# Optimization experiments

Measured on AMD Instinct MI355X. Metric: run time of the kernel, lower is better.

The kernel has to match this reference:

```python
import jax, jax.numpy as jnp
import numpy as np

NUM_USERS = 100000
NUM_ITEMS = 100000
DIM = 128
B = 8192
H = 200
ATTN_HID = 64


def setup_inputs() -> dict:
    key = jax.random.key(0)
    ks = jax.random.split(key, 10)
    user_ids = jax.random.randint(ks[0], (B,), 0, NUM_USERS)
    item_ids = jax.random.randint(ks[1], (B,), 0, NUM_ITEMS)
    user_history = jax.random.randint(ks[2], (B, H), 0, NUM_ITEMS)
    user_table = jax.random.normal(ks[3], (NUM_USERS, DIM), dtype=jnp.float32)
    item_table = jax.random.normal(ks[4], (NUM_ITEMS, DIM), dtype=jnp.float32)
    feature_interaction = jax.random.normal(ks[5], (DIM, DIM), dtype=jnp.float32)
    # attention MLP: Linear(2*DIM, 64) -> ReLU -> Linear(64, 1) -> Sigmoid
    lim1 = 1.0 / np.sqrt(2 * DIM)
    w1 = jax.random.uniform(ks[6], (2 * DIM, ATTN_HID), minval=-lim1, maxval=lim1, dtype=jnp.float32)
    b1 = jax.random.uniform(ks[7], (ATTN_HID,), minval=-lim1, maxval=lim1, dtype=jnp.float32)
    lim2 = 1.0 / np.sqrt(ATTN_HID)
    w2 = jax.random.uniform(ks[8], (ATTN_HID, 1), minval=-lim2, maxval=lim2, dtype=jnp.float32)
    b2 = jax.random.uniform(ks[9], (1,), minval=-lim2, maxval=lim2, dtype=jnp.float32)
    return {
        "user_ids": user_ids,
        "item_ids": item_ids,
        "user_history": user_history,
        "user_table": user_table,
        "item_table": item_table,
        "feature_interaction": feature_interaction,
        "w1": w1,
        "b1": b1,
        "w2": w2,
        "b2": b2,
    }


def reference(user_ids, item_ids, user_history, user_table, item_table,
              feature_interaction, w1, b1, w2, b2):
    user_emb = user_table[user_ids]          # [B, D]
    item_emb = item_table[item_ids]          # [B, D]
    # bilinear interaction: (user_emb @ W) . item_emb, summed over D -> [B, 1]
    interaction = jnp.sum((user_emb @ feature_interaction) * item_emb, axis=1, keepdims=True)
    # attention-weighted history pooling
    history_emb = item_table[user_history]   # [B, H, D]
    u = jnp.broadcast_to(user_emb[:, None, :], history_emb.shape)  # [B, H, D]
    attn_in = jnp.concatenate([u, history_emb], axis=-1)           # [B, H, 2D]
    h = jax.nn.relu(attn_in @ w1 + b1)                             # [B, H, 64]
    attn_w = jax.nn.sigmoid(h @ w2 + b2)                           # [B, H, 1]
    history_repr = jnp.sum(attn_w * history_emb, axis=1)           # [B, D]
    user_out = user_emb + history_repr
    return (user_out, item_emb, interaction)
```

## Files before the change

### kernel.cpp

```cpp
#include <hip/hip_runtime.h>
#include <math.h>

#define NB      8192
#define HLEN    200
#define DIM     128
#define AH      64
#define NITEMS  100000
#define NTILE   13
#define INTER_BLKS (NB / 32)

typedef __attribute__((ext_vector_type(4))) float f32x4;
typedef __attribute__((ext_vector_type(2))) float f32x2;
typedef __attribute__((ext_vector_type(4))) int   i32x4;
typedef __attribute__((ext_vector_type(8))) short bf16x8;
typedef unsigned int uint;

__device__ __forceinline__ unsigned short f2bf(float f) {
  uint u = __float_as_uint(f);
  u += 0x7fffu + ((u >> 16) & 1u);
  return (unsigned short)(u >> 16);
}
__device__ __forceinline__ float bf2f(unsigned short h) {
  return __uint_as_float(((uint)h) << 16);
}
__device__ __forceinline__ long pick64(const i32x4& v, int h) {
  return (long)(unsigned)v[2 * h] | ((long)(unsigned)v[2 * h + 1] << 32);
}
__device__ __forceinline__ i32x4 ldnt(const void* p) {
  return __builtin_nontemporal_load((const i32x4*)p);
}

__global__ __launch_bounds__(256)
void pre_kernel(const int* __restrict__ user_ids,
                const int* __restrict__ item_ids,
                const float* __restrict__ user_table,
                const float* __restrict__ item_table,
                const float* __restrict__ fi,
                const float* __restrict__ w1,
                unsigned char* __restrict__ tbl8,
                unsigned char* __restrict__ w1f8,
                float* __restrict__ out_item,
                float* __restrict__ out_inter) {
  const int t = threadIdx.x;
  if (blockIdx.x < INTER_BLKS) {
    __shared__ unsigned short fitb[DIM * 130];
    __shared__ float u4[4][DIM];
    __shared__ float red[4][4];
    for (int i = t; i < DIM * DIM; i += 256) {
      int d = i >> 7, e = i & 127;
      fitb[e * 130 + d] = f2bf(fi[i]);
    }
    const int col = t & 127;
    const int dh = t >> 7;
    const int lane = t & 63;
    const int wv = t >> 6;
    const int b0 = blockIdx.x * 32;
    const unsigned short* fr = &fitb[col * 130 + dh * 64];
    for (int grp = 0; grp < 8; ++grp) {
      __syncthreads();
      for (int i = t; i < 4 * DIM; i += 256) {
        int bi = i >> 7, d = i & 127;
        u4[bi][d] = user_table[(long)user_ids[b0 + grp * 4 + bi] * DIM + d];
      }
      __syncthreads();
      float a0 = 0.f, a1 = 0.f, a2 = 0.f, a3 = 0.f;
#pragma unroll 4
      for (int d = 0; d < 64; d += 4) {
        float f0 = bf2f(fr[d]), f1 = bf2f(fr[d + 1]), f2 = bf2f(fr[d + 2]), f3 = bf2f(fr[d + 3]);
        f32x4 q0 = *(const f32x4*)&u4[0][dh * 64 + d];
        f32x4 q1 = *(const f32x4*)&u4[1][dh * 64 + d];
        f32x4 q2 = *(const f32x4*)&u4[2][dh * 64 + d];
        f32x4 q3 = *(const f32x4*)&u4[3][dh * 64 + d];
        a0 = fmaf(f0, q0[0], a0); a0 = fmaf(f1, q0[1], a0); a0 = fmaf(f2, q0[2], a0); a0 = fmaf(f3, q0[3], a0);
        a1 = fmaf(f0, q1[0], a1); a1 = fmaf(f1, q1[1], a1); a1 = fmaf(f2, q1[2], a1); a1 = fmaf(f3, q1[3], a1);
        a2 = fmaf(f0, q2[0], a2); a2 = fmaf(f1, q2[1], a2); a2 = fmaf(f2, q2[2], a2); a2 = fmaf(f3, q2[3], a2);
        a3 = fmaf(f0, q3[0], a3); a3 = fmaf(f1, q3[1], a3); a3 = fmaf(f2, q3[2], a3); a3 = fmaf(f3, q3[3], a3);
      }
      const int bb = b0 + grp * 4;
      const float vv0 = item_table[(long)item_ids[bb + 0] * DIM + col];
      const float vv1 = item_table[(long)item_ids[bb + 1] * DIM + col];
      const float vv2 = item_table[(long)item_ids[bb + 2] * DIM + col];
      const float vv3 = item_table[(long)item_ids[bb + 3] * DIM + col];
      if (dh == 0) {
        out_item[(long)(bb + 0) * DIM + col] = vv0;
        out_item[(long)(bb + 1) * DIM + col] = vv1;
        out_item[(long)(bb + 2) * DIM + col] = vv2;
        out_item[(long)(bb + 3) * DIM + col] = vv3;
      }
      float p0 = a0 * vv0, p1 = a1 * vv1, p2 = a2 * vv2, p3 = a3 * vv3;
#pragma unroll
      for (int msk = 1; msk <= 32; msk <<= 1) {
        p0 += __shfl_xor(p0, msk);
        p1 += __shfl_xor(p1, msk);
        p2 += __shfl_xor(p2, msk);
        p3 += __shfl_xor(p3, msk);
      }
      if (lane == 0) { red[wv][0] = p0; red[wv][1] = p1; red[wv][2] = p2; red[wv][3] = p3; }
      __syncthreads();
      if (t < 4)
        out_inter[bb + t] = red[0][t] + red[1][t] + red[2][t] + red[3][t];
    }
  } else {
    const int cb = blockIdx.x - INTER_BLKS;
    const int cgrid = gridDim.x - INTER_BLKS;
    const long t0 = (long)cb * 256 + t;
    const long total4 = (long)NITEMS * DIM / 4;
    const long stride = (long)cgrid * 256;
    for (long i = t0; i < total4; i += stride) {
      f32x4 v = ((const f32x4*)item_table)[i];
      int p = __builtin_amdgcn_cvt_pk_fp8_f32(v[0], v[1], 0, false);
      p     = __builtin_amdgcn_cvt_pk_fp8_f32(v[2], v[3], p, true);
      ((int*)tbl8)[i] = p;
    }
    if (t0 < 16384) {
      int L = (int)t0;
      int j = L & 7, gg = (L >> 3) & 3, mm = (L >> 5) & 15;
      int nt = (L >> 9) & 3, s = (L >> 11) & 3, part = (L >> 13) & 1;
      int kg = part * 128 + (s >> 1) * 64 + gg * 16 + (s & 1) * 8 + j;
      float v = w1[kg * AH + nt * 16 + mm];
      int pk = __builtin_amdgcn_cvt_pk_fp8_f32(v, v, 0, false);
      w1f8[L] = (unsigned char)(pk & 0xff);
    }
  }
}

__global__ __launch_bounds__(256)
void main_kernel_fp8(const int* __restrict__ user_ids,
                     const int* __restrict__ user_history,
                     const float* __restrict__ user_table,
                     const unsigned char* __restrict__ tbl8,
                     const unsigned char* __restrict__ w1f8,
                     const float* __restrict__ b1,
                     const float* __restrict__ w2,
                     const float* __restrict__ b2,
                     float* __restrict__ out_user) {
  const int lane = threadIdx.x & 63;
  const int wave = threadIdx.x >> 6;
  const int b = blockIdx.x * 4 + wave;
  const int m = lane & 15;
  const int g = lane >> 4;

  const int uid = __builtin_amdgcn_readfirstlane(user_ids[b]);
  const float* urow = user_table + (long)uid * DIM;
  const int* hrow = user_history + (long)b * HLEN;

  int idxs[NTILE];
#pragma unroll
  for (int t = 0; t < NTILE; ++t) {
    int row = t * 16 + m;
    idxs[t] = (row < HLEN) ? hrow[row] : 0;
  }

  i32x4 pa[5][2];
#define LOADT(T, BUF)                                                          \
  {                                                                            \
    const unsigned char* p_ = tbl8 + ((long)idxs[T] << 7) + g * 16;            \
    pa[BUF][0] = ldnt(p_);                                                     \
    pa[BUF][1] = ldnt(p_ + 64);                                                \
  }
  LOADT(0, 0) LOADT(1, 1) LOADT(2, 2) LOADT(3, 3)

  i32x4 uf[2];
#pragma unroll
  for (int kb = 0; kb < 2; ++kb) {
    const float* up = urow + kb * 64 + g * 16;
    f32x4 q0 = *(const f32x4*)(up + 0);
    f32x4 q1 = *(const f32x4*)(up + 4);
    f32x4 q2 = *(const f32x4*)(up + 8);
    f32x4 q3 = *(const f32x4*)(up + 12);
    i32x4 d;
    d[0] = __builtin_amdgcn_cvt_pk_fp8_f32(q0[0], q0[1], 0, false);
    d[0] = __builtin_amdgcn_cvt_pk_fp8_f32(q0[2], q0[3], d[0], true);
    d[1] = __builtin_amdgcn_cvt_pk_fp8_f32(q1[0], q1[1], 0, false);
    d[1] = __builtin_amdgcn_cvt_pk_fp8_f32(q1[2], q1[3], d[1], true);
    d[2] = __builtin_amdgcn_cvt_pk_fp8_f32(q2[0], q2[1], 0, false);
    d[2] = __builtin_amdgcn_cvt_pk_fp8_f32(q2[2], q2[3], d[2], true);
    d[3] = __builtin_amdgcn_cvt_pk_fp8_f32(q3[0], q3[1], 0, false);
    d[3] = __builtin_amdgcn_cvt_pk_fp8_f32(q3[2], q3[3], d[3], true);
    uf[kb] = d;
  }

  const unsigned char* wtop = w1f8;
  const unsigned char* wbot = w1f8 + 8192;

  f32x4 accu[4];
#pragma unroll
  for (int nt = 0; nt < 4; ++nt) accu[nt] = (f32x4){0.f, 0.f, 0.f, 0.f};
#pragma unroll
  for (int s = 0; s < 4; ++s) {
    long a_s = pick64(uf[s >> 1], s & 1);
#pragma unroll
    for (int nt = 0; nt < 4; ++nt) {
      long bf = *(const long*)(wtop + ((s * 4 + nt) * 16 + m) * 32 + g * 8);
      accu[nt] = __builtin_amdgcn_mfma_f32_16x16x32_fp8_fp8(a_s, bf, accu[nt], 0, 0, 0);
    }
  }
  float ubreg[4], w2reg[4];
#pragma unroll
  for (int nt = 0; nt < 4; ++nt) {
    ubreg[nt] = accu[nt][0] + b1[nt * 16 + m];
    w2reg[nt] = w2[nt * 16 + m];
  }
  const float b2v = b2[0];

  long bfr[4][4];
#pragma unroll
  for (int s = 0; s < 4; ++s)
#pragma unroll
    for (int nt = 0; nt < 4; ++nt)
      bfr[s][nt] = *(const long*)(wbot + ((s * 4 + nt) * 16 + m) * 32 + g * 8);

  float arep[32];
#pragma unroll
  for (int c = 0; c < 32; ++c) arep[c] = 0.f;

#pragma unroll
  for (int t = 0; t < NTILE; ++t) {
    if (t + 4 < NTILE) LOADT(t + 4, (t + 4) % 5)
    const int cb = t % 5;

    f32x4 acc[4];
#pragma unroll
    for (int nt = 0; nt < 4; ++nt) acc[nt] = (f32x4){0.f, 0.f, 0.f, 0.f};
#pragma unroll
    for (int s = 0; s < 4; ++s) {
      long a_s = pick64(pa[cb][s >> 1], s & 1);
#pragma unroll
      for (int nt = 0; nt < 4; ++nt)
        acc[nt] = __builtin_amdgcn_mfma_f32_16x16x32_fp8_fp8(a_s, bfr[s][nt], acc[nt], 0, 0, 0);
    }

    float sums[4];
#pragma unroll
    for (int r = 0; r < 4; ++r) {
      float s = 0.f;
#pragma unroll
      for (int nt = 0; nt < 4; ++nt) {
        float h = fmaxf(acc[nt][r] + ubreg[nt], 0.f);
        s = fmaf(h, w2reg[nt], s);
      }
      s += __shfl_xor(s, 1);
      s += __shfl_xor(s, 2);
      s += __shfl_xor(s, 4);
      s += __shfl_xor(s, 8);
      sums[r] = s;
    }
    const int q = m & 3;
    float keep = (q == 0) ? sums[0] : (q == 1) ? sums[1] : (q == 2) ? sums[2] : sums[3];
    float sv = __shfl(keep, ((m >> 2) << 4) | m);
    float attw = 1.f / (1.f + __expf(-(sv + b2v)));
    if (t * 16 + m >= HLEN) attw = 0.f;

#pragma unroll
    for (int kb = 0; kb < 2; ++kb)
#pragma unroll
      for (int d = 0; d < 4; ++d) {
        f32x2 lo = __builtin_amdgcn_cvt_pk_f32_fp8(pa[cb][kb][d], false);
        f32x2 hi = __builtin_amdgcn_cvt_pk_f32_fp8(pa[cb][kb][d], true);
        const int base = kb * 16 + d * 4;
        arep[base + 0] = fmaf(attw, lo[0], arep[base + 0]);
        arep[base + 1] = fmaf(attw, lo[1], arep[base + 1]);
        arep[base + 2] = fmaf(attw, hi[0], arep[base + 2]);
        arep[base + 3] = fmaf(attw, hi[1], arep[base + 3]);
      }
  }
#undef LOADT

#pragma unroll
  for (int c = 0; c < 32; ++c) {
    arep[c] += __shfl_xor(arep[c], 1);
    arep[c] += __shfl_xor(arep[c], 2);
    arep[c] += __shfl_xor(arep[c], 4);
    arep[c] += __shfl_xor(arep[c], 8);
  }
  if (m == 0) {
#pragma unroll
    for (int kb = 0; kb < 2; ++kb)
#pragma unroll
      for (int i4 = 0; i4 < 4; ++i4) {
        const int col = kb * 64 + g * 16 + i4 * 4;
        f32x4 uv = *(const f32x4*)(urow + col);
        f32x4 o;
#pragma unroll
        for (int qq = 0; qq < 4; ++qq) o[qq] = uv[qq] + arep[kb * 16 + i4 * 4 + qq];
        *(f32x4*)(out_user + (long)b * DIM + col) = o;
      }
  }
}

__global__ __launch_bounds__(256)
void main_fallback(const int* __restrict__ user_ids,
                   const int* __restrict__ user_history,
                   const float* __restrict__ user_table,
                   const float* __restrict__ item_table,
                   const float* __restrict__ w1,
                   const float* __restrict__ b1,
                   const float* __restrict__ w2,
                   const float* __restrict__ b2,
                   float* __restrict__ out_user) {
  const int lane = threadIdx.x & 63;
  const int wave = threadIdx.x >> 6;
  const int b = blockIdx.x * 4 + wave;
  const int m = lane & 15, g = lane >> 4;
  const int uid = __builtin_amdgcn_readfirstlane(user_ids[b]);
  const float* urow = user_table + (long)uid * DIM;
  float upj = b1[lane];
#pragma unroll 8
  for (int d = 0; d < DIM; ++d) upj = fmaf(urow[d], w1[d * AH + lane], upj);
  bf16x8 bfr[4][4];
#pragma unroll
  for (int ks = 0; ks < 4; ++ks)
#pragma unroll
    for (int nt = 0; nt < 4; ++nt) {
      bf16x8 bv;
#pragma unroll
      for (int j = 0; j < 8; ++j)
        bv[j] = (short)f2bf(w1[(DIM + ks * 32 + g * 8 + j) * AH + nt * 16 + m]);
      bfr[ks][nt] = bv;
    }
  float ubreg[4], w2reg[4];
#pragma unroll
  for (int nt = 0; nt < 4; ++nt) {
    ubreg[nt] = __shfl(upj, nt * 16 + m);
    w2reg[nt] = w2[nt * 16 + m];
  }
  const float b2v = b2[0];
  float arep[32];
#pragma unroll
  for (int c = 0; c < 32; ++c) arep[c] = 0.f;
  const int* hrow = user_history + (long)b * HLEN;
  for (int t = 0; t < NTILE; ++t) {
    const int row = t * 16 + m;
    const int idx = (row < HLEN) ? hrow[row] : 0;
    bf16x8 a[4];
    const float* rp = item_table + (long)idx * DIM;
#pragma unroll
    for (int ks = 0; ks < 4; ++ks) {
      f32x4 lo = *(const f32x4*)(rp + ks * 32 + g * 8);
      f32x4 hi = *(const f32x4*)(rp + ks * 32 + g * 8 + 4);
      bf16x8 av;
      av[0] = (short)f2bf(lo[0]); av[1] = (short)f2bf(lo[1]);
      av[2] = (short)f2bf(lo[2]); av[3] = (short)f2bf(lo[3]);
      av[4] = (short)f2bf(hi[0]); av[5] = (short)f2bf(hi[1]);
      av[6] = (short)f2bf(hi[2]); av[7] = (short)f2bf(hi[3]);
      a[ks] = av;
    }
    f32x4 acc[4];
#pragma unroll
    for (int nt = 0; nt < 4; ++nt) acc[nt] = (f32x4){0.f, 0.f, 0.f, 0.f};
#pragma unroll
    for (int ks = 0; ks < 4; ++ks)
#pragma unroll
      for (int nt = 0; nt < 4; ++nt)
        acc[nt] = __builtin_amdgcn_mfma_f32_16x16x32_bf16(a[ks], bfr[ks][nt], acc[nt], 0, 0, 0);
    float sums[4];
#pragma unroll
    for (int r = 0; r < 4; ++r) {
      float s = 0.f;
#pragma unroll
      for (int nt = 0; nt < 4; ++nt) {
        float h = fmaxf(acc[nt][r] + ubreg[nt], 0.f);
        s = fmaf(h, w2reg[nt], s);
      }
      s += __shfl_xor(s, 1); s += __shfl_xor(s, 2);
      s += __shfl_xor(s, 4); s += __shfl_xor(s, 8);
      sums[r] = s;
    }
    const int q = m & 3;
    float keep = (q == 0) ? sums[0] : (q == 1) ? sums[1] : (q == 2) ? sums[2] : sums[3];
    float sv = __shfl(keep, ((m >> 2) << 4) | m);
    float attw = 1.f / (1.f + __expf(-(sv + b2v)));
    if (row >= HLEN) attw = 0.f;
#pragma unroll
    for (int ks = 0; ks < 4; ++ks)
#pragma unroll
      for (int j = 0; j < 8; ++j)
        arep[ks * 8 + j] = fmaf(attw, bf2f((unsigned short)a[ks][j]), arep[ks * 8 + j]);
  }
#pragma unroll
  for (int c = 0; c < 32; ++c) {
    arep[c] += __shfl_xor(arep[c], 1);
    arep[c] += __shfl_xor(arep[c], 2);
    arep[c] += __shfl_xor(arep[c], 4);
    arep[c] += __shfl_xor(arep[c], 8);
  }
  if (m == 0) {
#pragma unroll
    for (int ks = 0; ks < 4; ++ks)
#pragma unroll
      for (int j = 0; j < 8; ++j) {
        const int col = ks * 32 + g * 8 + j;
        out_user[(long)b * DIM + col] = urow[col] + arep[ks * 8 + j];
      }
  }
}

extern "C" void kernel_launch(void* const* d_in, const int* in_sizes, int n_in,
                              void* d_out, int out_size, void* d_ws, size_t ws_size,
                              hipStream_t stream) {
  const int*   user_ids     = (const int*)d_in[0];
  const int*   item_ids     = (const int*)d_in[1];
  const int*   user_history = (const int*)d_in[2];
  const float* user_table   = (const float*)d_in[3];
  const float* item_table   = (const float*)d_in[4];
  const float* fi           = (const float*)d_in[5];
  const float* w1           = (const float*)d_in[6];
  const float* b1           = (const float*)d_in[7];
  const float* w2           = (const float*)d_in[8];
  const float* b2           = (const float*)d_in[9];

  float* out       = (float*)d_out;
  float* out_user  = out;
  float* out_item  = out + (size_t)NB * DIM;
  float* out_inter = out + (size_t)2 * NB * DIM;

  const size_t need = (size_t)NITEMS * DIM + 16384;
  if (ws_size >= need) {
    unsigned char* tbl8 = (unsigned char*)d_ws;
    unsigned char* w1f8 = tbl8 + (size_t)NITEMS * DIM;
    pre_kernel<<<INTER_BLKS + 1024, 256, 0, stream>>>(user_ids, item_ids, user_table,
        item_table, fi, w1, tbl8, w1f8, out_item, out_inter);
    main_kernel_fp8<<<NB / 4, 256, 0, stream>>>(user_ids, user_history, user_table,
        tbl8, w1f8, b1, w2, b2, out_user);
  } else {
    main_fallback<<<NB / 4, 256, 0, stream>>>(user_ids, user_history, user_table,
        item_table, w1, b1, w2, b2, out_user);
    pre_kernel<<<INTER_BLKS, 256, 0, stream>>>(user_ids, item_ids, user_table,
        item_table, fi, w1, nullptr, nullptr, out_item, out_inter);
  }
}
```

Measured before the change: 109.1 us.

## Stage history gathers into LDS via async global_load_lds with explicit waitcnt pipeline

The main kernel now gathers the fp8 history rows straight into a swizzled, 5-deep per-wave LDS ring using global_load_lds, instead of holding them in registers. Consumption is paced by explicit vmcnt waits, and loads are issued as each tile is consumed. This frees VGPRs and overlaps the gathers with MFMA work. W1 fragments and biases are hoisted up front, and b1 is folded into the accumulator init. The pre-kernel now uses one block per 4 batch rows instead of 32, so the interaction blocks each rebuild the transposed bf16 feature matrix in LDS, which adds redundant preload work.

```diff
diff --git a/kernel.cpp b/kernel.cpp
--- a/kernel.cpp
+++ b/kernel.cpp
@@ -7,7 +7,8 @@
 #define AH      64
 #define NITEMS  100000
 #define NTILE   13
-#define INTER_BLKS (NB / 32)
+#define GRP_BLKS (NB / 4)
+#define CONV_BLKS 1024
 
 typedef __attribute__((ext_vector_type(4))) float f32x4;
 typedef __attribute__((ext_vector_type(2))) float f32x2;
@@ -26,8 +27,10 @@
 __device__ __forceinline__ long pick64(const i32x4& v, int h) {
   return (long)(unsigned)v[2 * h] | ((long)(unsigned)v[2 * h + 1] << 32);
 }
-__device__ __forceinline__ i32x4 ldnt(const void* p) {
-  return __builtin_nontemporal_load((const i32x4*)p);
+__device__ __forceinline__ void gld16(const unsigned char* g, unsigned char* l) {
+  __builtin_amdgcn_global_load_lds(
+      (const __attribute__((address_space(1))) unsigned int*)g,
+      (__attribute__((address_space(3))) unsigned int*)l, 16, 0, 0);
 }
 
 __global__ __launch_bounds__(256)
@@ -42,7 +45,7 @@
                 float* __restrict__ out_item,
                 float* __restrict__ out_inter) {
   const int t = threadIdx.x;
-  if (blockIdx.x < INTER_BLKS) {
+  if (blockIdx.x < GRP_BLKS) {
     __shared__ unsigned short fitb[DIM * 130];
     __shared__ float u4[4][DIM];
     __shared__ float red[4][4];
@@ -54,58 +57,53 @@
     const int dh = t >> 7;
     const int lane = t & 63;
     const int wv = t >> 6;
-    const int b0 = blockIdx.x * 32;
+    const int bb = blockIdx.x * 4;
+    for (int i = t; i < 4 * DIM; i += 256) {
+      int bi = i >> 7, d = i & 127;
+      u4[bi][d] = user_table[(long)user_ids[bb + bi] * DIM + d];
+    }
+    __syncthreads();
     const unsigned short* fr = &fitb[col * 130 + dh * 64];
-    for (int grp = 0; grp < 8; ++grp) {
-      __syncthreads();
-      for (int i = t; i < 4 * DIM; i += 256) {
-        int bi = i >> 7, d = i & 127;
-        u4[bi][d] = user_table[(long)user_ids[b0 + grp * 4 + bi] * DIM + d];
-      }
-      __syncthreads();
-      float a0 = 0.f, a1 = 0.f, a2 = 0.f, a3 = 0.f;
+    float a0 = 0.f, a1 = 0.f, a2 = 0.f, a3 = 0.f;
 #pragma unroll 4
-      for (int d = 0; d < 64; d += 4) {
-        float f0 = bf2f(fr[d]), f1 = bf2f(fr[d + 1]), f2 = bf2f(fr[d + 2]), f3 = bf2f(fr[d + 3]);
-        f32x4 q0 = *(const f32x4*)&u4[0][dh * 64 + d];
-        f32x4 q1 = *(const f32x4*)&u4[1][dh * 64 + d];
-        f32x4 q2 = *(const f32x4*)&u4[2][dh * 64 + d];
-        f32x4 q3 = *(const f32x4*)&u4[3][dh * 64 + d];
-        a0 = fmaf(f0, q0[0], a0); a0 = fmaf(f1, q0[1], a0); a0 = fmaf(f2, q0[2], a0); a0 = fmaf(f3, q0[3], a0);
-        a1 = fmaf(f0, q1[0], a1); a1 = fmaf(f1, q1[1], a1); a1 = fmaf(f2, q1[2], a1); a1 = fmaf(f3, q1[3], a1);
-        a2 = fmaf(f0, q2[0], a2); a2 = fmaf(f1, q2[1], a2); a2 = fmaf(f2, q2[2], a2); a2 = fmaf(f3, q2[3], a2);
-        a3 = fmaf(f0, q3[0], a3); a3 = fmaf(f1, q3[1], a3); a3 = fmaf(f2, q3[2], a3); a3 = fmaf(f3, q3[3], a3);
-      }
-      const int bb = b0 + grp * 4;
-      const float vv0 = item_table[(long)item_ids[bb + 0] * DIM + col];
-      const float vv1 = item_table[(long)item_ids[bb + 1] * DIM + col];
-      const float vv2 = item_table[(long)item_ids[bb + 2] * DIM + col];
-      const float vv3 = item_table[(long)item_ids[bb + 3] * DIM + col];
-      if (dh == 0) {
-        out_item[(long)(bb + 0) * DIM + col] = vv0;
-        out_item[(long)(bb + 1) * DIM + col] = vv1;
-        out_item[(long)(bb + 2) * DIM + col] = vv2;
-        out_item[(long)(bb + 3) * DIM + col] = vv3;
-      }
-      float p0 = a0 * vv0, p1 = a1 * vv1, p2 = a2 * vv2, p3 = a3 * vv3;
-#pragma unroll
-      for (int msk = 1; msk <= 32; msk <<= 1) {
-        p0 += __shfl_xor(p0, msk);
-        p1 += __shfl_xor(p1, msk);
-        p2 += __shfl_xor(p2, msk);
-        p3 += __shfl_xor(p3, msk);
-      }
-      if (lane == 0) { red[wv][0] = p0; red[wv][1] = p1; red[wv][2] = p2; red[wv][3] = p3; }
-      __syncthreads();
-      if (t < 4)
-        out_inter[bb + t] = red[0][t] + red[1][t] + red[2][t] + red[3][t];
-    }
+    for (int d = 0; d < 64; d += 4) {
+      float f0 = bf2f(fr[d]), f1 = bf2f(fr[d + 1]), f2 = bf2f(fr[d + 2]), f3 = bf2f(fr[d + 3]);
+      f32x4 q0 = *(const f32x4*)&u4[0][dh * 64 + d];
+      f32x4 q1 = *(const f32x4*)&u4[1][dh * 64 + d];
+      f32x4 q2 = *(const f32x4*)&u4[2][dh * 64 + d];
+      f32x4 q3 = *(const f32x4*)&u4[3][dh * 64 + d];
+      a0 = fmaf(f0, q0[0], a0); a0 = fmaf(f1, q0[1], a0); a0 = fmaf(f2, q0[2], a0); a0 = fmaf(f3, q0[3], a0);
+      a1 = fmaf(f0, q1[0], a1); a1 = fmaf(f1, q1[1], a1); a1 = fmaf(f2, q1[2], a1); a1 = fmaf(f3, q1[3], a1);
+      a2 = fmaf(f0, q2[0], a2); a2 = fmaf(f1, q2[1], a2); a2 = fmaf(f2, q2[2], a2); a2 = fmaf(f3, q2[3], a2);
+      a3 = fmaf(f0, q3[0], a3); a3 = fmaf(f1, q3[1], a3); a3 = fmaf(f2, q3[2], a3); a3 = fmaf(f3, q3[3], a3);
+    }
+    const float vv0 = item_table[(long)item_ids[bb + 0] * DIM + col];
+    const float vv1 = item_table[(long)item_ids[bb + 1] * DIM + col];
+    const float vv2 = item_table[(long)item_ids[bb + 2] * DIM + col];
+    const float vv3 = item_table[(long)item_ids[bb + 3] * DIM + col];
+    if (dh == 0) {
+      out_item[(long)(bb + 0) * DIM + col] = vv0;
+      out_item[(long)(bb + 1) * DIM + col] = vv1;
+      out_item[(long)(bb + 2) * DIM + col] = vv2;
+      out_item[(long)(bb + 3) * DIM + col] = vv3;
+    }
+    float p0 = a0 * vv0, p1 = a1 * vv1, p2 = a2 * vv2, p3 = a3 * vv3;
+#pragma unroll
+    for (int msk = 1; msk <= 32; msk <<= 1) {
+      p0 += __shfl_xor(p0, msk);
+      p1 += __shfl_xor(p1, msk);
+      p2 += __shfl_xor(p2, msk);
+      p3 += __shfl_xor(p3, msk);
+    }
+    if (lane == 0) { red[wv][0] = p0; red[wv][1] = p1; red[wv][2] = p2; red[wv][3] = p3; }
+    __syncthreads();
+    if (t < 4)
+      out_inter[bb + t] = red[0][t] + red[1][t] + red[2][t] + red[3][t];
   } else {
-    const int cb = blockIdx.x - INTER_BLKS;
-    const int cgrid = gridDim.x - INTER_BLKS;
+    const int cb = blockIdx.x - GRP_BLKS;
     const long t0 = (long)cb * 256 + t;
     const long total4 = (long)NITEMS * DIM / 4;
-    const long stride = (long)cgrid * 256;
+    const long stride = (long)CONV_BLKS * 256;
     for (long i = t0; i < total4; i += stride) {
       f32x4 v = ((const f32x4*)item_table)[i];
       int p = __builtin_amdgcn_cvt_pk_fp8_f32(v[0], v[1], 0, false);
@@ -134,11 +132,13 @@
                      const float* __restrict__ w2,
                      const float* __restrict__ b2,
                      float* __restrict__ out_user) {
+  __shared__ unsigned char stg[4][5 * 2048];
   const int lane = threadIdx.x & 63;
   const int wave = threadIdx.x >> 6;
   const int b = blockIdx.x * 4 + wave;
   const int m = lane & 15;
   const int g = lane >> 4;
+  unsigned char* mystg = &stg[wave][0];
 
   const int uid = __builtin_amdgcn_readfirstlane(user_ids[b]);
   const float* urow = user_table + (long)uid * DIM;
@@ -151,37 +151,56 @@
     idxs[t] = (row < HLEN) ? hrow[row] : 0;
   }
 
-  i32x4 pa[5][2];
-#define LOADT(T, BUF)                                                          \
-  {                                                                            \
-    const unsigned char* p_ = tbl8 + ((long)idxs[T] << 7) + g * 16;            \
-    pa[BUF][0] = ldnt(p_);                                                     \
-    pa[BUF][1] = ldnt(p_ + 64);                                                \
-  }
-  LOADT(0, 0) LOADT(1, 1) LOADT(2, 2) LOADT(3, 3)
-
-  i32x4 uf[2];
-#pragma unroll
-  for (int kb = 0; kb < 2; ++kb) {
-    const float* up = urow + kb * 64 + g * 16;
-    f32x4 q0 = *(const f32x4*)(up + 0);
-    f32x4 q1 = *(const f32x4*)(up + 4);
-    f32x4 q2 = *(const f32x4*)(up + 8);
-    f32x4 q3 = *(const f32x4*)(up + 12);
-    i32x4 d;
-    d[0] = __builtin_amdgcn_cvt_pk_fp8_f32(q0[0], q0[1], 0, false);
-    d[0] = __builtin_amdgcn_cvt_pk_fp8_f32(q0[2], q0[3], d[0], true);
-    d[1] = __builtin_amdgcn_cvt_pk_fp8_f32(q1[0], q1[1], 0, false);
-    d[1] = __builtin_amdgcn_cvt_pk_fp8_f32(q1[2], q1[3], d[1], true);
-    d[2] = __builtin_amdgcn_cvt_pk_fp8_f32(q2[0], q2[1], 0, false);
-    d[2] = __builtin_amdgcn_cvt_pk_fp8_f32(q2[2], q2[3], d[2], true);
-    d[3] = __builtin_amdgcn_cvt_pk_fp8_f32(q3[0], q3[1], 0, false);
-    d[3] = __builtin_amdgcn_cvt_pk_fp8_f32(q3[2], q3[3], d[3], true);
-    uf[kb] = d;
-  }
+  f32x4 uq[8];
+#pragma unroll
+  for (int kb = 0; kb < 2; ++kb)
+#pragma unroll
+    for (int j = 0; j < 4; ++j)
+      uq[kb * 4 + j] = *(const f32x4*)(urow + kb * 64 + g * 16 + 4 * j);
 
   const unsigned char* wtop = w1f8;
   const unsigned char* wbot = w1f8 + 8192;
+  long wt[4][4], bfr[4][4];
+#pragma unroll
+  for (int s = 0; s < 4; ++s)
+#pragma unroll
+    for (int nt = 0; nt < 4; ++nt) {
+      wt[s][nt]  = *(const long*)(wtop + ((s * 4 + nt) * 16 + m) * 32 + g * 8);
+      bfr[s][nt] = *(const long*)(wbot + ((s * 4 + nt) * 16 + m) * 32 + g * 8);
+    }
+  float b1reg[4], w2reg[4];
+#pragma unroll
+  for (int nt = 0; nt < 4; ++nt) {
+    b1reg[nt] = b1[nt * 16 + m];
+    w2reg[nt] = w2[nt * 16 + m];
+  }
+  const float b2v = b2[0];
+
+  const unsigned swg = (unsigned)(((lane & 7) ^ (lane >> 3)) << 4);
+#define LOADT(T)                                                               \
+  {                                                                            \
+    int r0_ = __shfl(idxs[T], lane >> 3);                                      \
+    int r1_ = __shfl(idxs[T], 8 + (lane >> 3));                                \
+    unsigned char* l0_ = mystg + ((T) % 5) * 2048;                             \
+    gld16(tbl8 + ((long)r0_ << 7) + swg, l0_);                                 \
+    gld16(tbl8 + ((long)r1_ << 7) + swg, l0_ + 1024);                          \
+  }
+  LOADT(0) LOADT(1) LOADT(2) LOADT(3) LOADT(4)
+
+  i32x4 uf[2];
+#pragma unroll
+  for (int kb = 0; kb < 2; ++kb) {
+    i32x4 d;
+    d[0] = __builtin_amdgcn_cvt_pk_fp8_f32(uq[kb*4+0][0], uq[kb*4+0][1], 0, false);
+    d[0] = __builtin_amdgcn_cvt_pk_fp8_f32(uq[kb*4+0][2], uq[kb*4+0][3], d[0], true);
+    d[1] = __builtin_amdgcn_cvt_pk_fp8_f32(uq[kb*4+1][0], uq[kb*4+1][1], 0, false);
+    d[1] = __builtin_amdgcn_cvt_pk_fp8_f32(uq[kb*4+1][2], uq[kb*4+1][3], d[1], true);
+    d[2] = __builtin_amdgcn_cvt_pk_fp8_f32(uq[kb*4+2][0], uq[kb*4+2][1], 0, false);
+    d[2] = __builtin_amdgcn_cvt_pk_fp8_f32(uq[kb*4+2][2], uq[kb*4+2][3], d[2], true);
+    d[3] = __builtin_amdgcn_cvt_pk_fp8_f32(uq[kb*4+3][0], uq[kb*4+3][1], 0, false);
+    d[3] = __builtin_amdgcn_cvt_pk_fp8_f32(uq[kb*4+3][2], uq[kb*4+3][3], d[3], true);
+    uf[kb] = d;
+  }
 
   f32x4 accu[4];
 #pragma unroll
@@ -190,80 +209,83 @@
   for (int s = 0; s < 4; ++s) {
     long a_s = pick64(uf[s >> 1], s & 1);
 #pragma unroll
-    for (int nt = 0; nt < 4; ++nt) {
-      long bf = *(const long*)(wtop + ((s * 4 + nt) * 16 + m) * 32 + g * 8);
-      accu[nt] = __builtin_amdgcn_mfma_f32_16x16x32_fp8_fp8(a_s, bf, accu[nt], 0, 0, 0);
-    }
-  }
-  float ubreg[4], w2reg[4];
-#pragma unroll
-  for (int nt = 0; nt < 4; ++nt) {
-    ubreg[nt] = accu[nt][0] + b1[nt * 16 + m];
-    w2reg[nt] = w2[nt * 16 + m];
-  }
-  const float b2v = b2[0];
-
-  long bfr[4][4];
-#pragma unroll
-  for (int s = 0; s < 4; ++s)
-#pragma unroll
     for (int nt = 0; nt < 4; ++nt)
-      bfr[s][nt] = *(const long*)(wbot + ((s * 4 + nt) * 16 + m) * 32 + g * 8);
+      accu[nt] = __builtin_amdgcn_mfma_f32_16x16x32_fp8_fp8(a_s, wt[s][nt], accu[nt], 0, 0, 0);
+  }
+  float ubreg[4];
+#pragma unroll
+  for (int nt = 0; nt < 4; ++nt) ubreg[nt] = accu[nt][0] + b1reg[nt];
 
   float arep[32];
 #pragma unroll
   for (int c = 0; c < 32; ++c) arep[c] = 0.f;
 
-#pragma unroll
-  for (int t = 0; t < NTILE; ++t) {
-    if (t + 4 < NTILE) LOADT(t + 4, (t + 4) % 5)
-    const int cb = t % 5;
-
-    f32x4 acc[4];
-#pragma unroll
-    for (int nt = 0; nt < 4; ++nt) acc[nt] = (f32x4){0.f, 0.f, 0.f, 0.f};
-#pragma unroll
-    for (int s = 0; s < 4; ++s) {
-      long a_s = pick64(pa[cb][s >> 1], s & 1);
-#pragma unroll
-      for (int nt = 0; nt < 4; ++nt)
-        acc[nt] = __builtin_amdgcn_mfma_f32_16x16x32_fp8_fp8(a_s, bfr[s][nt], acc[nt], 0, 0, 0);
-    }
-
-    float sums[4];
-#pragma unroll
-    for (int r = 0; r < 4; ++r) {
-      float s = 0.f;
-#pragma unroll
-      for (int nt = 0; nt < 4; ++nt) {
-        float h = fmaxf(acc[nt][r] + ubreg[nt], 0.f);
-        s = fmaf(h, w2reg[nt], s);
-      }
-      s += __shfl_xor(s, 1);
-      s += __shfl_xor(s, 2);
-      s += __shfl_xor(s, 4);
-      s += __shfl_xor(s, 8);
-      sums[r] = s;
-    }
-    const int q = m & 3;
-    float keep = (q == 0) ? sums[0] : (q == 1) ? sums[1] : (q == 2) ? sums[2] : sums[3];
-    float sv = __shfl(keep, ((m >> 2) << 4) | m);
-    float attw = 1.f / (1.f + __expf(-(sv + b2v)));
-    if (t * 16 + m >= HLEN) attw = 0.f;
-
-#pragma unroll
-    for (int kb = 0; kb < 2; ++kb)
-#pragma unroll
-      for (int d = 0; d < 4; ++d) {
-        f32x2 lo = __builtin_amdgcn_cvt_pk_f32_fp8(pa[cb][kb][d], false);
-        f32x2 hi = __builtin_amdgcn_cvt_pk_f32_fp8(pa[cb][kb][d], true);
-        const int base = kb * 16 + d * 4;
-        arep[base + 0] = fmaf(attw, lo[0], arep[base + 0]);
-        arep[base + 1] = fmaf(attw, lo[1], arep[base + 1]);
-        arep[base + 2] = fmaf(attw, hi[0], arep[base + 2]);
-        arep[base + 3] = fmaf(attw, hi[1], arep[base + 3]);
-      }
-  }
+  const unsigned sw0 = (unsigned)((g ^ (m & 7)) << 4);
+
+#define STEP(T, WN, ISS)                                                       \
+  {                                                                            \
+    asm volatile("s_waitcnt vmcnt(" WN ")" ::: "memory");                      \
+    __builtin_amdgcn_sched_barrier(0);                                         \
+    const unsigned char* rp_ = mystg + ((T) % 5) * 2048 + (m << 7);            \
+    i32x4 pa0 = *(const i32x4*)(rp_ + sw0);                                    \
+    i32x4 pa1 = *(const i32x4*)(rp_ + (sw0 ^ 64));                             \
+    f32x4 acc[4];                                                              \
+    _Pragma("unroll")                                                          \
+    for (int nt = 0; nt < 4; ++nt)                                             \
+      acc[nt] = (f32x4){ubreg[nt], ubreg[nt], ubreg[nt], ubreg[nt]};           \
+    _Pragma("unroll")                                                          \
+    for (int s = 0; s < 4; ++s) {                                              \
+      long a_s = pick64((s < 2) ? pa0 : pa1, s & 1);                           \
+      _Pragma("unroll")                                                        \
+      for (int nt = 0; nt < 4; ++nt)                                           \
+        acc[nt] = __builtin_amdgcn_mfma_f32_16x16x32_fp8_fp8(a_s, bfr[s][nt], acc[nt], 0, 0, 0); \
+    }                                                                          \
+    float sums[4];                                                             \
+    _Pragma("unroll")                                                          \
+    for (int r = 0; r < 4; ++r) {                                              \
+      float s_ = fmaxf(acc[0][r], 0.f) * w2reg[0];                             \
+      s_ = fmaf(fmaxf(acc[1][r], 0.f), w2reg[1], s_);                          \
+      s_ = fmaf(fmaxf(acc[2][r], 0.f), w2reg[2], s_);                          \
+      s_ = fmaf(fmaxf(acc[3][r], 0.f), w2reg[3], s_);                          \
+      s_ += __shfl_xor(s_, 1);                                                 \
+      s_ += __shfl_xor(s_, 2);                                                 \
+      s_ += __shfl_xor(s_, 4);                                                 \
+      s_ += __shfl_xor(s_, 8);                                                 \
+      sums[r] = s_;                                                            \
+    }                                                                          \
+    const int q_ = m & 3;                                                      \
+    float keep_ = (q_ == 0) ? sums[0] : (q_ == 1) ? sums[1]                    \
+                 : (q_ == 2) ? sums[2] : sums[3];                              \
+    float sv_ = __shfl(keep_, ((m >> 2) << 4) | m);                            \
+    float attw = 1.f / (1.f + __expf(-(sv_ + b2v)));                           \
+    if ((T) * 16 + m >= HLEN) attw = 0.f;                                      \
+    _Pragma("unroll")                                                          \
+    for (int d = 0; d < 4; ++d) {                                              \
+      f32x2 lo0 = __builtin_amdgcn_cvt_pk_f32_fp8(pa0[d], false);              \
+      f32x2 hi0 = __builtin_amdgcn_cvt_pk_f32_fp8(pa0[d], true);               \
+      arep[d * 4 + 0] = fmaf(attw, lo0[0], arep[d * 4 + 0]);                   \
+      arep[d * 4 + 1] = fmaf(attw, lo0[1], arep[d * 4 + 1]);                   \
+      arep[d * 4 + 2] = fmaf(attw, hi0[0], arep[d * 4 + 2]);                   \
+      arep[d * 4 + 3] = fmaf(attw, hi0[1], arep[d * 4 + 3]);                   \
+      f32x2 lo1 = __builtin_amdgcn_cvt_pk_f32_fp8(pa1[d], false);              \
+      f32x2 hi1 = __builtin_amdgcn_cvt_pk_f32_fp8(pa1[d], true);               \
+      arep[16 + d * 4 + 0] = fmaf(attw, lo1[0], arep[16 + d * 4 + 0]);         \
+      arep[16 + d * 4 + 1] = fmaf(attw, lo1[1], arep[16 + d * 4 + 1]);         \
+      arep[16 + d * 4 + 2] = fmaf(attw, hi1[0], arep[16 + d * 4 + 2]);         \
+      arep[16 + d * 4 + 3] = fmaf(attw, hi1[1], arep[16 + d * 4 + 3]);         \
+    }                                                                          \
+    if ((ISS) < NTILE) {                                                       \
+      asm volatile("s_waitcnt lgkmcnt(0)" ::: "memory");                       \
+      __builtin_amdgcn_sched_barrier(0);                                       \
+      LOADT(ISS);                                                              \
+    }                                                                          \
+  }
+
+  STEP(0, "8", 5)  STEP(1, "8", 6)  STEP(2, "8", 7)  STEP(3, "8", 8)
+  STEP(4, "8", 9)  STEP(5, "8", 10) STEP(6, "8", 11) STEP(7, "8", 12)
+  STEP(8, "8", 13) STEP(9, "6", 13) STEP(10, "4", 13) STEP(11, "2", 13)
+  STEP(12, "0", 13)
+#undef STEP
 #undef LOADT
 
 #pragma unroll
@@ -418,14 +440,14 @@
   if (ws_size >= need) {
     unsigned char* tbl8 = (unsigned char*)d_ws;
     unsigned char* w1f8 = tbl8 + (size_t)NITEMS * DIM;
-    pre_kernel<<<INTER_BLKS + 1024, 256, 0, stream>>>(user_ids, item_ids, user_table,
+    pre_kernel<<<GRP_BLKS + CONV_BLKS, 256, 0, stream>>>(user_ids, item_ids, user_table,
         item_table, fi, w1, tbl8, w1f8, out_item, out_inter);
     main_kernel_fp8<<<NB / 4, 256, 0, stream>>>(user_ids, user_history, user_table,
         tbl8, w1f8, b1, w2, b2, out_user);
   } else {
     main_fallback<<<NB / 4, 256, 0, stream>>>(user_ids, user_history, user_table,
         item_table, w1, b1, w2, b2, out_user);
-    pre_kernel<<<INTER_BLKS, 256, 0, stream>>>(user_ids, item_ids, user_table,
+    pre_kernel<<<GRP_BLKS, 256, 0, stream>>>(user_ids, item_ids, user_table,
         item_table, fi, w1, nullptr, nullptr, out_item, out_inter);
   }
 }
```

Result: faster. 99.44 us (-8.9%).

## Split history pooling across two waves per row and regrid interaction blocks

Applied to the files above, without the earlier changes.

The main fp8 kernel now gives each batch row two waves, each covering about half of the history tiles. The two halves are combined through a small shared-memory buffer, so there are twice as many waves, each with a shorter serial tile loop. Accumulation switches to packed two-wide float math, and launch bounds and prefetch depth are adjusted. The interaction part of the prep kernel now uses one block per four rows instead of one per thirty-two, for more parallelism. The cost is that each block redoes the transpose and conversion of the feature matrix into shared memory, and each history wave repeats the per-row setup work.

```diff
diff --git a/kernel.cpp b/kernel.cpp
--- a/kernel.cpp
+++ b/kernel.cpp
@@ -7,7 +7,9 @@
 #define AH      64
 #define NITEMS  100000
 #define NTILE   13
-#define INTER_BLKS (NB / 32)
+#define WTILES  7
+#define GRP_BLKS (NB / 4)
+#define CONV_BLKS 1024
 
 typedef __attribute__((ext_vector_type(4))) float f32x4;
 typedef __attribute__((ext_vector_type(2))) float f32x2;
@@ -42,7 +44,7 @@
                 float* __restrict__ out_item,
                 float* __restrict__ out_inter) {
   const int t = threadIdx.x;
-  if (blockIdx.x < INTER_BLKS) {
+  if (blockIdx.x < GRP_BLKS) {
     __shared__ unsigned short fitb[DIM * 130];
     __shared__ float u4[4][DIM];
     __shared__ float red[4][4];
@@ -54,58 +56,53 @@
     const int dh = t >> 7;
     const int lane = t & 63;
     const int wv = t >> 6;
-    const int b0 = blockIdx.x * 32;
+    const int bb = blockIdx.x * 4;
+    for (int i = t; i < 4 * DIM; i += 256) {
+      int bi = i >> 7, d = i & 127;
+      u4[bi][d] = user_table[(long)user_ids[bb + bi] * DIM + d];
+    }
+    __syncthreads();
     const unsigned short* fr = &fitb[col * 130 + dh * 64];
-    for (int grp = 0; grp < 8; ++grp) {
-      __syncthreads();
-      for (int i = t; i < 4 * DIM; i += 256) {
-        int bi = i >> 7, d = i & 127;
-        u4[bi][d] = user_table[(long)user_ids[b0 + grp * 4 + bi] * DIM + d];
-      }
-      __syncthreads();
-      float a0 = 0.f, a1 = 0.f, a2 = 0.f, a3 = 0.f;
+    float a0 = 0.f, a1 = 0.f, a2 = 0.f, a3 = 0.f;
 #pragma unroll 4
-      for (int d = 0; d < 64; d += 4) {
-        float f0 = bf2f(fr[d]), f1 = bf2f(fr[d + 1]), f2 = bf2f(fr[d + 2]), f3 = bf2f(fr[d + 3]);
-        f32x4 q0 = *(const f32x4*)&u4[0][dh * 64 + d];
-        f32x4 q1 = *(const f32x4*)&u4[1][dh * 64 + d];
-        f32x4 q2 = *(const f32x4*)&u4[2][dh * 64 + d];
-        f32x4 q3 = *(const f32x4*)&u4[3][dh * 64 + d];
-        a0 = fmaf(f0, q0[0], a0); a0 = fmaf(f1, q0[1], a0); a0 = fmaf(f2, q0[2], a0); a0 = fmaf(f3, q0[3], a0);
-        a1 = fmaf(f0, q1[0], a1); a1 = fmaf(f1, q1[1], a1); a1 = fmaf(f2, q1[2], a1); a1 = fmaf(f3, q1[3], a1);
-        a2 = fmaf(f0, q2[0], a2); a2 = fmaf(f1, q2[1], a2); a2 = fmaf(f2, q2[2], a2); a2 = fmaf(f3, q2[3], a2);
-        a3 = fmaf(f0, q3[0], a3); a3 = fmaf(f1, q3[1], a3); a3 = fmaf(f2, q3[2], a3); a3 = fmaf(f3, q3[3], a3);
-      }
-      const int bb = b0 + grp * 4;
-      const float vv0 = item_table[(long)item_ids[bb + 0] * DIM + col];
-      const float vv1 = item_table[(long)item_ids[bb + 1] * DIM + col];
-      const float vv2 = item_table[(long)item_ids[bb + 2] * DIM + col];
-      const float vv3 = item_table[(long)item_ids[bb + 3] * DIM + col];
-      if (dh == 0) {
-        out_item[(long)(bb + 0) * DIM + col] = vv0;
-        out_item[(long)(bb + 1) * DIM + col] = vv1;
-        out_item[(long)(bb + 2) * DIM + col] = vv2;
-        out_item[(long)(bb + 3) * DIM + col] = vv3;
-      }
-      float p0 = a0 * vv0, p1 = a1 * vv1, p2 = a2 * vv2, p3 = a3 * vv3;
-#pragma unroll
-      for (int msk = 1; msk <= 32; msk <<= 1) {
-        p0 += __shfl_xor(p0, msk);
-        p1 += __shfl_xor(p1, msk);
-        p2 += __shfl_xor(p2, msk);
-        p3 += __shfl_xor(p3, msk);
-      }
-      if (lane == 0) { red[wv][0] = p0; red[wv][1] = p1; red[wv][2] = p2; red[wv][3] = p3; }
-      __syncthreads();
-      if (t < 4)
-        out_inter[bb + t] = red[0][t] + red[1][t] + red[2][t] + red[3][t];
-    }
+    for (int d = 0; d < 64; d += 4) {
+      float f0 = bf2f(fr[d]), f1 = bf2f(fr[d + 1]), f2 = bf2f(fr[d + 2]), f3 = bf2f(fr[d + 3]);
+      f32x4 q0 = *(const f32x4*)&u4[0][dh * 64 + d];
+      f32x4 q1 = *(const f32x4*)&u4[1][dh * 64 + d];
+      f32x4 q2 = *(const f32x4*)&u4[2][dh * 64 + d];
+      f32x4 q3 = *(const f32x4*)&u4[3][dh * 64 + d];
+      a0 = fmaf(f0, q0[0], a0); a0 = fmaf(f1, q0[1], a0); a0 = fmaf(f2, q0[2], a0); a0 = fmaf(f3, q0[3], a0);
+      a1 = fmaf(f0, q1[0], a1); a1 = fmaf(f1, q1[1], a1); a1 = fmaf(f2, q1[2], a1); a1 = fmaf(f3, q1[3], a1);
+      a2 = fmaf(f0, q2[0], a2); a2 = fmaf(f1, q2[1], a2); a2 = fmaf(f2, q2[2], a2); a2 = fmaf(f3, q2[3], a2);
+      a3 = fmaf(f0, q3[0], a3); a3 = fmaf(f1, q3[1], a3); a3 = fmaf(f2, q3[2], a3); a3 = fmaf(f3, q3[3], a3);
+    }
+    const float vv0 = item_table[(long)item_ids[bb + 0] * DIM + col];
+    const float vv1 = item_table[(long)item_ids[bb + 1] * DIM + col];
+    const float vv2 = item_table[(long)item_ids[bb + 2] * DIM + col];
+    const float vv3 = item_table[(long)item_ids[bb + 3] * DIM + col];
+    if (dh == 0) {
+      out_item[(long)(bb + 0) * DIM + col] = vv0;
+      out_item[(long)(bb + 1) * DIM + col] = vv1;
+      out_item[(long)(bb + 2) * DIM + col] = vv2;
+      out_item[(long)(bb + 3) * DIM + col] = vv3;
+    }
+    float p0 = a0 * vv0, p1 = a1 * vv1, p2 = a2 * vv2, p3 = a3 * vv3;
+#pragma unroll
+    for (int msk = 1; msk <= 32; msk <<= 1) {
+      p0 += __shfl_xor(p0, msk);
+      p1 += __shfl_xor(p1, msk);
+      p2 += __shfl_xor(p2, msk);
+      p3 += __shfl_xor(p3, msk);
+    }
+    if (lane == 0) { red[wv][0] = p0; red[wv][1] = p1; red[wv][2] = p2; red[wv][3] = p3; }
+    __syncthreads();
+    if (t < 4)
+      out_inter[bb + t] = red[0][t] + red[1][t] + red[2][t] + red[3][t];
   } else {
-    const int cb = blockIdx.x - INTER_BLKS;
-    const int cgrid = gridDim.x - INTER_BLKS;
+    const int cb = blockIdx.x - GRP_BLKS;
     const long t0 = (long)cb * 256 + t;
     const long total4 = (long)NITEMS * DIM / 4;
-    const long stride = (long)cgrid * 256;
+    const long stride = (long)CONV_BLKS * 256;
     for (long i = t0; i < total4; i += stride) {
       f32x4 v = ((const f32x4*)item_table)[i];
       int p = __builtin_amdgcn_cvt_pk_fp8_f32(v[0], v[1], 0, false);
@@ -124,7 +121,7 @@
   }
 }
 
-__global__ __launch_bounds__(256)
+__global__ __launch_bounds__(256, 4)
 void main_kernel_fp8(const int* __restrict__ user_ids,
                      const int* __restrict__ user_history,
                      const float* __restrict__ user_table,
@@ -134,9 +131,12 @@
                      const float* __restrict__ w2,
                      const float* __restrict__ b2,
                      float* __restrict__ out_user) {
+  __shared__ float comb[2][128];
   const int lane = threadIdx.x & 63;
   const int wave = threadIdx.x >> 6;
-  const int b = blockIdx.x * 4 + wave;
+  const int bslot = wave >> 1;
+  const int h = wave & 1;
+  const int b = blockIdx.x * 2 + bslot;
   const int m = lane & 15;
   const int g = lane >> 4;
 
@@ -144,21 +144,21 @@
   const float* urow = user_table + (long)uid * DIM;
   const int* hrow = user_history + (long)b * HLEN;
 
-  int idxs[NTILE];
-#pragma unroll
-  for (int t = 0; t < NTILE; ++t) {
-    int row = t * 16 + m;
+  int idxs[WTILES];
+#pragma unroll
+  for (int t = 0; t < WTILES; ++t) {
+    int row = (h * WTILES + t) * 16 + m;
     idxs[t] = (row < HLEN) ? hrow[row] : 0;
   }
 
-  i32x4 pa[5][2];
+  i32x4 pa[4][2];
 #define LOADT(T, BUF)                                                          \
   {                                                                            \
     const unsigned char* p_ = tbl8 + ((long)idxs[T] << 7) + g * 16;            \
     pa[BUF][0] = ldnt(p_);                                                     \
     pa[BUF][1] = ldnt(p_ + 64);                                                \
   }
-  LOADT(0, 0) LOADT(1, 1) LOADT(2, 2) LOADT(3, 3)
+  LOADT(0, 0) LOADT(1, 1) LOADT(2, 2)
 
   i32x4 uf[2];
 #pragma unroll
@@ -210,14 +210,14 @@
     for (int nt = 0; nt < 4; ++nt)
       bfr[s][nt] = *(const long*)(wbot + ((s * 4 + nt) * 16 + m) * 32 + g * 8);
 
-  float arep[32];
-#pragma unroll
-  for (int c = 0; c < 32; ++c) arep[c] = 0.f;
-
-#pragma unroll
-  for (int t = 0; t < NTILE; ++t) {
-    if (t + 4 < NTILE) LOADT(t + 4, (t + 4) % 5)
-    const int cb = t % 5;
+  f32x2 arep2[16];
+#pragma unroll
+  for (int c = 0; c < 16; ++c) arep2[c] = (f32x2){0.f, 0.f};
+
+#pragma unroll
+  for (int t = 0; t < WTILES; ++t) {
+    if (t + 3 < WTILES) LOADT(t + 3, (t + 3) & 3)
+    const int cb = t & 3;
 
     f32x4 acc[4];
 #pragma unroll
@@ -236,8 +236,8 @@
       float s = 0.f;
 #pragma unroll
       for (int nt = 0; nt < 4; ++nt) {
-        float h = fmaxf(acc[nt][r] + ubreg[nt], 0.f);
-        s = fmaf(h, w2reg[nt], s);
+        float hh = fmaxf(acc[nt][r] + ubreg[nt], 0.f);
+        s = fmaf(hh, w2reg[nt], s);
       }
       s += __shfl_xor(s, 1);
       s += __shfl_xor(s, 2);
@@ -249,7 +249,8 @@
     float keep = (q == 0) ? sums[0] : (q == 1) ? sums[1] : (q == 2) ? sums[2] : sums[3];
     float sv = __shfl(keep, ((m >> 2) << 4) | m);
     float attw = 1.f / (1.f + __expf(-(sv + b2v)));
-    if (t * 16 + m >= HLEN) attw = 0.f;
+    if ((h * WTILES + t) * 16 + m >= HLEN) attw = 0.f;
+    const f32x2 aw2 = (f32x2){attw, attw};
 
 #pragma unroll
     for (int kb = 0; kb < 2; ++kb)
@@ -257,23 +258,35 @@
       for (int d = 0; d < 4; ++d) {
         f32x2 lo = __builtin_amdgcn_cvt_pk_f32_fp8(pa[cb][kb][d], false);
         f32x2 hi = __builtin_amdgcn_cvt_pk_f32_fp8(pa[cb][kb][d], true);
-        const int base = kb * 16 + d * 4;
-        arep[base + 0] = fmaf(attw, lo[0], arep[base + 0]);
-        arep[base + 1] = fmaf(attw, lo[1], arep[base + 1]);
-        arep[base + 2] = fmaf(attw, hi[0], arep[base + 2]);
-        arep[base + 3] = fmaf(attw, hi[1], arep[base + 3]);
+        const int base = kb * 8 + d * 2;
+        arep2[base + 0] = arep2[base + 0] + aw2 * lo;
+        arep2[base + 1] = arep2[base + 1] + aw2 * hi;
       }
   }
 #undef LOADT
 
 #pragma unroll
-  for (int c = 0; c < 32; ++c) {
-    arep[c] += __shfl_xor(arep[c], 1);
-    arep[c] += __shfl_xor(arep[c], 2);
-    arep[c] += __shfl_xor(arep[c], 4);
-    arep[c] += __shfl_xor(arep[c], 8);
-  }
-  if (m == 0) {
+  for (int c = 0; c < 16; ++c) {
+#pragma unroll
+    for (int e = 0; e < 2; ++e) {
+      float v = arep2[c][e];
+      v += __shfl_xor(v, 1);
+      v += __shfl_xor(v, 2);
+      v += __shfl_xor(v, 4);
+      v += __shfl_xor(v, 8);
+      arep2[c][e] = v;
+    }
+  }
+
+  if (h == 1 && m == 0) {
+#pragma unroll
+    for (int c = 0; c < 16; ++c) {
+      comb[bslot][g * 32 + 2 * c + 0] = arep2[c][0];
+      comb[bslot][g * 32 + 2 * c + 1] = arep2[c][1];
+    }
+  }
+  __syncthreads();
+  if (h == 0 && m == 0) {
 #pragma unroll
     for (int kb = 0; kb < 2; ++kb)
 #pragma unroll
@@ -282,7 +295,10 @@
         f32x4 uv = *(const f32x4*)(urow + col);
         f32x4 o;
 #pragma unroll
-        for (int qq = 0; qq < 4; ++qq) o[qq] = uv[qq] + arep[kb * 16 + i4 * 4 + qq];
+        for (int qq = 0; qq < 4; ++qq) {
+          const int c2 = kb * 16 + i4 * 4 + qq;
+          o[qq] = uv[qq] + arep2[c2 >> 1][c2 & 1] + comb[bslot][g * 32 + c2];
+        }
         *(f32x4*)(out_user + (long)b * DIM + col) = o;
       }
   }
@@ -359,8 +375,8 @@
       float s = 0.f;
 #pragma unroll
       for (int nt = 0; nt < 4; ++nt) {
-        float h = fmaxf(acc[nt][r] + ubreg[nt], 0.f);
-        s = fmaf(h, w2reg[nt], s);
+        float hh = fmaxf(acc[nt][r] + ubreg[nt], 0.f);
+        s = fmaf(hh, w2reg[nt], s);
       }
       s += __shfl_xor(s, 1); s += __shfl_xor(s, 2);
       s += __shfl_xor(s, 4); s += __shfl_xor(s, 8);
@@ -418,14 +434,14 @@
   if (ws_size >= need) {
     unsigned char* tbl8 = (unsigned char*)d_ws;
     unsigned char* w1f8 = tbl8 + (size_t)NITEMS * DIM;
-    pre_kernel<<<INTER_BLKS + 1024, 256, 0, stream>>>(user_ids, item_ids, user_table,
+    pre_kernel<<<GRP_BLKS + CONV_BLKS, 256, 0, stream>>>(user_ids, item_ids, user_table,
         item_table, fi, w1, tbl8, w1f8, out_item, out_inter);
-    main_kernel_fp8<<<NB / 4, 256, 0, stream>>>(user_ids, user_history, user_table,
+    main_kernel_fp8<<<NB / 2, 256, 0, stream>>>(user_ids, user_history, user_table,
         tbl8, w1f8, b1, w2, b2, out_user);
   } else {
     main_fallback<<<NB / 4, 256, 0, stream>>>(user_ids, user_history, user_table,
         item_table, w1, b1, w2, b2, out_user);
-    pre_kernel<<<INTER_BLKS, 256, 0, stream>>>(user_ids, item_ids, user_table,
+    pre_kernel<<<GRP_BLKS, 256, 0, stream>>>(user_ids, item_ids, user_table,
         item_table, fi, w1, nullptr, nullptr, out_item, out_inter);
   }
 }
```

Result: slower. 127.7 us (+17.1%).
